# Kernel optimization log

Hardware: AMD Instinct MI355X
Metric: run time of the kernel (lower is better)

The kernel has to match this reference:

```python
import jax, jax.numpy as jnp
import numpy as np

L = 4            # num_layers
N_GENES = 2048   # col_dim: rows of x, PPI graph nodes
N_CELLS = 2048   # row_dim: cols of x, KNN graph nodes
E_KNN = 30720    # ~k=15 per cell
E_PPI = 65536    # ~avg degree 32 per gene
NEG_SLOPE = 0.01 # nn.LeakyReLU default


def setup_inputs() -> dict:
    key = jax.random.key(0)
    ks = jax.random.split(key, 9)
    x = jax.random.normal(ks[0], (N_GENES, N_CELLS), jnp.float32)
    knn_edge_index = jax.random.randint(ks[1], (2, E_KNN), 0, N_CELLS)
    ppi_edge_index = jax.random.randint(ks[2], (2, E_PPI), 0, N_GENES)
    s_c = 1.0 / np.sqrt(N_GENES)  # cols side feature dim = col_dim
    s_r = 1.0 / np.sqrt(N_CELLS)  # rows side feature dim = row_dim
    col_Wl = jax.random.normal(ks[3], (L, N_GENES, N_GENES), jnp.float32) * s_c
    col_bl = jnp.zeros((L, N_GENES), jnp.float32)
    col_Wr = jax.random.normal(ks[4], (L, N_GENES, N_GENES), jnp.float32) * s_c
    row_Wl = jax.random.normal(ks[5], (L, N_CELLS, N_CELLS), jnp.float32) * s_r
    row_bl = jnp.zeros((L, N_CELLS), jnp.float32)
    row_Wr = jax.random.normal(ks[6], (L, N_CELLS, N_CELLS), jnp.float32) * s_r
    return dict(x=x, knn_edge_index=knn_edge_index, ppi_edge_index=ppi_edge_index,
                col_Wl=col_Wl, col_bl=col_bl, col_Wr=col_Wr,
                row_Wl=row_Wl, row_bl=row_bl, row_Wr=row_Wr)


def _sage(h, edge_index, Wl, bl, Wr):
    # PyG SAGEConv (mean aggr): out = lin_l(mean_{j->i} h_j) + lin_r(h_i)
    src, tgt = edge_index[0], edge_index[1]
    n = h.shape[0]
    summed = jax.ops.segment_sum(h[src], tgt, num_segments=n)          # [n, d]
    cnt = jax.ops.segment_sum(jnp.ones((src.shape[0],), h.dtype), tgt, num_segments=n)
    mean = summed / jnp.maximum(cnt, 1.0)[:, None]
    return mean @ Wl + bl + h @ Wr


def reference(x, knn_edge_index, ppi_edge_index,
              col_Wl, col_bl, col_Wr, row_Wl, row_bl, row_Wr):
    # Dropout is identity in eval mode; layer = SAGEConv -> LeakyReLU on both sides.
    h = x  # [N_GENES, N_CELLS]
    for i in range(L):
        # cols side: operate on h.T [N_CELLS, N_GENES] over KNN graph
        h = jax.nn.leaky_relu(_sage(h.T, knn_edge_index, col_Wl[i], col_bl[i], col_Wr[i]),
                              negative_slope=NEG_SLOPE).T
        # rows side: operate on h [N_GENES, N_CELLS] over PPI graph
        h = jax.nn.leaky_relu(_sage(h, ppi_edge_index, row_Wl[i], row_bl[i], row_Wr[i]),
                              negative_slope=NEG_SLOPE)
    return h
```

## Files before the change

kernel.cpp:

```cpp
#include <hip/hip_runtime.h>
#include <stdint.h>

#define NSZ 2048
#define NLAYERS 4

typedef __attribute__((ext_vector_type(4))) float f32x4;
typedef __attribute__((ext_vector_type(4))) _Float16 f16x4;
typedef __attribute__((ext_vector_type(8))) _Float16 f16x8;

__device__ __forceinline__ void gload_lds16(const void* g, void* l) {
  __builtin_amdgcn_global_load_lds((const __attribute__((address_space(1))) void*)g,
                                   (__attribute__((address_space(3))) void*)l, 16, 0, 0);
}

__global__ void k_zero(int* __restrict__ p, int n) {
  int i = blockIdx.x * 256 + threadIdx.x;
  if (i < n) p[i] = 0;
}

__global__ void k_count(const int* __restrict__ tgt, int E, int* __restrict__ cnt) {
  int e = blockIdx.x * 256 + threadIdx.x;
  if (e < E) atomicAdd(&cnt[tgt[e] & (NSZ - 1)], 1);
}

__global__ __launch_bounds__(1024) void k_scan(
    const int* __restrict__ cntA, int* __restrict__ offA, int* __restrict__ curA,
    float* __restrict__ invA, int EA,
    const int* __restrict__ cntB, int* __restrict__ offB, int* __restrict__ curB,
    float* __restrict__ invB, int EB) {
  const int* cnt; int* off; int* cur; float* inv; int E;
  if (blockIdx.x == 0) { cnt = cntA; off = offA; cur = curA; inv = invA; E = EA; }
  else                 { cnt = cntB; off = offB; cur = curB; inv = invB; E = EB; }
  __shared__ int sa[2048], sb[2048];
  int t = threadIdx.x;
  sa[t] = cnt[t]; sa[t + 1024] = cnt[t + 1024];
  __syncthreads();
  int* s = sa; int* d = sb;
  for (int dd = 1; dd < 2048; dd <<= 1) {
    for (int i = t; i < 2048; i += 1024)
      d[i] = s[i] + ((i >= dd) ? s[i - dd] : 0);
    __syncthreads();
    int* tmp = s; s = d; d = tmp;
  }
  for (int i = t; i < 2048; i += 1024) {
    int o = (i == 0) ? 0 : s[i - 1];
    off[i] = o; cur[i] = o;
    int c = cnt[i];
    inv[i] = 1.0f / (float)((c > 1) ? c : 1);
  }
  if (t == 0) off[2048] = E;
}

__global__ void k_fill(const int* __restrict__ src, const int* __restrict__ tgt, int E,
                       int* __restrict__ cur, int* __restrict__ srcs) {
  int e = blockIdx.x * 256 + threadIdx.x;
  if (e < E) {
    int p = atomicAdd(&cur[tgt[e] & (NSZ - 1)], 1);
    if (p >= 0 && p < E) srcs[p] = src[e] & (NSZ - 1);
  }
}

__global__ __launch_bounds__(256) void k_transpose(const float* __restrict__ s,
                                                   float* __restrict__ d) {
  __shared__ float tile[64][65];
  const int tid = threadIdx.x;
  const int r0 = blockIdx.y << 6, c0 = blockIdx.x << 6;
#pragma unroll
  for (int it = 0; it < 4; ++it) {
    int e = it * 256 + tid;
    int r = e >> 4;
    int c = (e & 15) << 2;
    f32x4 v = *(const f32x4*)&s[(size_t)(r0 + r) * NSZ + c0 + c];
#pragma unroll
    for (int j = 0; j < 4; ++j) tile[r][c + j] = v[j];
  }
  __syncthreads();
#pragma unroll
  for (int it = 0; it < 4; ++it) {
    int e = it * 256 + tid;
    int r = e >> 4;
    int c = (e & 15) << 2;
    f32x4 v;
#pragma unroll
    for (int j = 0; j < 4; ++j) v[j] = tile[c + j][r];
    *(f32x4*)&d[(size_t)(c0 + r) * NSZ + r0 + c] = v;
  }
}

__global__ __launch_bounds__(256) void k_cvtA(const float* __restrict__ X,
                                              _Float16* __restrict__ Ah,
                                              _Float16* __restrict__ Al) {
  int idx = blockIdx.x * 256 + threadIdx.x;
  int m = idx >> 9;
  int c = idx & 511;
  f32x4 v = *(const f32x4*)&X[((size_t)m << 11) + (c << 2)];
  f16x4 hi, lo;
#pragma unroll
  for (int j = 0; j < 4; ++j) {
    float x = v[j];
    _Float16 h = (_Float16)x;
    hi[j] = h;
    lo[j] = (_Float16)(x - (float)h);
  }
  size_t rowb = (size_t)m << 12;
  int byte = (c << 3) ^ (((m >> 1) & 3) << 4);
  *(f16x4*)((char*)Ah + rowb + byte) = hi;
  *(f16x4*)((char*)Al + rowb + byte) = lo;
}

__global__ __launch_bounds__(256) void k_cvtB(const float* __restrict__ Wl,
                                              const float* __restrict__ Wr,
                                              _Float16* __restrict__ Bh,
                                              _Float16* __restrict__ Bl) {
  __shared__ float tile[64][65];
  const float* W = blockIdx.z ? Wr : Wl;
  const int nbase = blockIdx.z ? NSZ : 0;
  const int tid = threadIdx.x;
  const int k0 = blockIdx.y << 6;
  const int n0 = blockIdx.x << 6;
#pragma unroll
  for (int it = 0; it < 4; ++it) {
    int e = it * 256 + tid;
    int r = e >> 4;
    int c = (e & 15) << 2;
    f32x4 v = *(const f32x4*)&W[(size_t)(k0 + r) * NSZ + n0 + c];
#pragma unroll
    for (int j = 0; j < 4; ++j) tile[r][c + j] = v[j];
  }
  __syncthreads();
#pragma unroll
  for (int it = 0; it < 4; ++it) {
    int e = it * 256 + tid;
    int r = e >> 4;
    int c4 = (e & 15) << 2;
    f16x4 hi, lo;
#pragma unroll
    for (int j = 0; j < 4; ++j) {
      float x = tile[c4 + j][r];
      _Float16 h = (_Float16)x;
      hi[j] = h;
      lo[j] = (_Float16)(x - (float)h);
    }
    int n = nbase + n0 + r;
    size_t rowb = (size_t)n << 12;
    int byte = ((k0 + c4) << 1) ^ (((n >> 1) & 3) << 4);
    *(f16x4*)((char*)Bh + rowb + byte) = hi;
    *(f16x4*)((char*)Bl + rowb + byte) = lo;
  }
}

__global__ __launch_bounds__(256, 2) void k_gemm16(
    const _Float16* __restrict__ Ah, const _Float16* __restrict__ Al,
    const _Float16* __restrict__ Bh, const _Float16* __restrict__ Bl,
    float* __restrict__ C) {
  __shared__ __align__(128) _Float16 lds[4][128][32];
  const int tid = threadIdx.x;
  const int w = tid >> 6;
  const int lane = tid & 63;
  const int bm = blockIdx.x & 15;
  const int bn = blockIdx.x >> 4;
  const int m0 = bm << 7;
  const int n0 = bn << 7;
  const int wm = (w & 1) << 6;
  const int wn = (w >> 1) << 6;

  f32x4 acc[4][4];
#pragma unroll
  for (int i = 0; i < 4; ++i)
#pragma unroll
    for (int j = 0; j < 4; ++j)
#pragma unroll
      for (int r = 0; r < 4; ++r) acc[i][j][r] = 0.f;

  const int srow0 = (w << 5) + (lane >> 2);
  const int scol = (lane & 3) << 3;
  const int l15 = lane & 15;
  const int ks16 = (lane >> 4) << 4;

  for (int k0 = 0; k0 < NSZ; k0 += 32) {
    __syncthreads();
#pragma unroll
    for (int q = 0; q < 2; ++q) {
      const int r = srow0 + (q << 4);
      const int dr = ((w << 1) + q) << 4;
      gload_lds16(&Ah[(size_t)(m0 + r) * NSZ + k0 + scol], &lds[0][dr][0]);
      gload_lds16(&Al[(size_t)(m0 + r) * NSZ + k0 + scol], &lds[1][dr][0]);
      gload_lds16(&Bh[(size_t)(n0 + r) * NSZ + k0 + scol], &lds[2][dr][0]);
      gload_lds16(&Bl[(size_t)(n0 + r) * NSZ + k0 + scol], &lds[3][dr][0]);
    }
    __syncthreads();

    f16x8 afh[4], afl[4], bfh[4], bfl[4];
#pragma unroll
    for (int f = 0; f < 4; ++f) {
      const int ra = wm + (f << 4) + l15;
      const int ca = ks16 ^ (((ra >> 1) & 3) << 4);
      afh[f] = *(const f16x8*)((const char*)&lds[0][ra][0] + ca);
      afl[f] = *(const f16x8*)((const char*)&lds[1][ra][0] + ca);
      const int rb = wn + (f << 4) + l15;
      const int cb = ks16 ^ (((rb >> 1) & 3) << 4);
      bfh[f] = *(const f16x8*)((const char*)&lds[2][rb][0] + cb);
      bfl[f] = *(const f16x8*)((const char*)&lds[3][rb][0] + cb);
    }
#pragma unroll
    for (int i = 0; i < 4; ++i)
#pragma unroll
      for (int j = 0; j < 4; ++j) {
        acc[i][j] = __builtin_amdgcn_mfma_f32_16x16x32_f16(afh[i], bfh[j], acc[i][j], 0, 0, 0);
        acc[i][j] = __builtin_amdgcn_mfma_f32_16x16x32_f16(afh[i], bfl[j], acc[i][j], 0, 0, 0);
        acc[i][j] = __builtin_amdgcn_mfma_f32_16x16x32_f16(afl[i], bfh[j], acc[i][j], 0, 0, 0);
      }
  }

  const int cr = (lane >> 4) << 2;
#pragma unroll
  for (int i = 0; i < 4; ++i)
#pragma unroll
    for (int j = 0; j < 4; ++j) {
      float* Cp = &C[(size_t)(m0 + wm + (i << 4) + cr) * 4096 + n0 + wn + (j << 4) + l15];
#pragma unroll
      for (int r = 0; r < 4; ++r) Cp[(size_t)r * 4096] = acc[i][j][r];
    }
}

__global__ __launch_bounds__(256) void k_fuse(const float* __restrict__ Cb,
                                              const int* __restrict__ off,
                                              const int* __restrict__ srcs,
                                              const float* __restrict__ inv,
                                              const float* __restrict__ bias,
                                              float* __restrict__ out,
                                              int transpose_out, int E) {
  __shared__ float tile[64][65];
  const int tid = threadIdx.x;
  const int w = tid >> 6;
  const int lane = tid & 63;
  const int t0 = blockIdx.y << 6;
  const int f0 = blockIdx.x << 6;
  const int fc = f0 + lane;
  const float b = bias[fc];

  for (int it = 0; it < 16; ++it) {
    int lt = (w << 4) + it;
    int c = t0 + lt;
    int e0 = off[c], e1 = off[c + 1];
    if (e1 > E) e1 = E;
    if (e0 < 0) e0 = 0;
    float acc = 0.f;
    int e = e0;
    while (e + 8 <= e1) {
      float p[8];
#pragma unroll
      for (int q = 0; q < 8; ++q)
        p[q] = Cb[(size_t)(srcs[e + q] & (NSZ - 1)) * 4096 + fc];
#pragma unroll
      for (int q = 0; q < 8; ++q) acc += p[q];
      e += 8;
    }
    while (e < e1) { acc += Cb[(size_t)(srcs[e] & (NSZ - 1)) * 4096 + fc]; ++e; }
    float val = acc * inv[c] + Cb[(size_t)c * 4096 + 2048 + fc] + b;
    val = (val > 0.f) ? val : 0.01f * val;
    tile[lt][lane] = val;
  }
  __syncthreads();
  for (int it = 0; it < 4; ++it) {
    int f = it * 256 + tid;
    int r = f >> 4;
    int c4 = (f & 15) << 2;
    f32x4 v;
    if (transpose_out) {
#pragma unroll
      for (int j = 0; j < 4; ++j) v[j] = tile[c4 + j][r];
      *(f32x4*)&out[(size_t)(f0 + r) * NSZ + t0 + c4] = v;
    } else {
#pragma unroll
      for (int j = 0; j < 4; ++j) v[j] = tile[r][c4 + j];
      *(f32x4*)&out[(size_t)(t0 + r) * NSZ + f0 + c4] = v;
    }
  }
}

extern "C" void kernel_launch(void* const* d_in, const int* in_sizes, int n_in,
                              void* d_out, int out_size, void* d_ws, size_t ws_size,
                              hipStream_t stream) {
  (void)n_in; (void)out_size; (void)ws_size;
  const float* x      = (const float*)d_in[0];
  const int*   knn    = (const int*)d_in[1];
  const int*   ppi    = (const int*)d_in[2];
  const float* col_Wl = (const float*)d_in[3];
  const float* col_bl = (const float*)d_in[4];
  const float* col_Wr = (const float*)d_in[5];
  const float* row_Wl = (const float*)d_in[6];
  const float* row_bl = (const float*)d_in[7];
  const float* row_Wr = (const float*)d_in[8];
  float* out = (float*)d_out;
  const int E_knn = in_sizes[1] / 2;
  const int E_ppi = in_sizes[2] / 2;
  const size_t NN = (size_t)NSZ * NSZ;

  char* ws = (char*)d_ws;
  size_t off_b = 0;
  int*   cnt_knn = (int*)(ws + off_b);   off_b += 2048 * 4;
  int*   cnt_ppi = (int*)(ws + off_b);   off_b += 2048 * 4;
  int*   off_knn = (int*)(ws + off_b);   off_b += 2064 * 4;
  int*   off_ppi = (int*)(ws + off_b);   off_b += 2064 * 4;
  int*   cur_knn = (int*)(ws + off_b);   off_b += 2048 * 4;
  int*   cur_ppi = (int*)(ws + off_b);   off_b += 2048 * 4;
  float* inv_knn = (float*)(ws + off_b); off_b += 2048 * 4;
  float* inv_ppi = (float*)(ws + off_b); off_b += 2048 * 4;
  int*   src_knn = (int*)(ws + off_b);   off_b += (size_t)((E_knn + 63) & ~63) * 4;
  int*   src_ppi = (int*)(ws + off_b);   off_b += (size_t)((E_ppi + 63) & ~63) * 4;
  off_b = (off_b + 255) & ~(size_t)255;
  float*     Cbuf = (float*)(ws + off_b);     off_b += NN * 2 * 4;
  _Float16*  Ahw  = (_Float16*)(ws + off_b);  off_b += NN * 2;
  _Float16*  Alw  = (_Float16*)(ws + off_b);  off_b += NN * 2;
  _Float16*  Bhw  = (_Float16*)(ws + off_b);  off_b += NN * 2 * 2;
  _Float16*  Blw  = (_Float16*)(ws + off_b);  off_b += NN * 2 * 2;
  float* state = out;

  k_zero<<<16, 256, 0, stream>>>(cnt_knn, 4096);
  k_count<<<(E_knn + 255) / 256, 256, 0, stream>>>(knn + E_knn, E_knn, cnt_knn);
  k_count<<<(E_ppi + 255) / 256, 256, 0, stream>>>(ppi + E_ppi, E_ppi, cnt_ppi);
  k_scan<<<2, 1024, 0, stream>>>(cnt_knn, off_knn, cur_knn, inv_knn, E_knn,
                                 cnt_ppi, off_ppi, cur_ppi, inv_ppi, E_ppi);
  k_fill<<<(E_knn + 255) / 256, 256, 0, stream>>>(knn, knn + E_knn, E_knn, cur_knn, src_knn);
  k_fill<<<(E_ppi + 255) / 256, 256, 0, stream>>>(ppi, ppi + E_ppi, E_ppi, cur_ppi, src_ppi);

  {
    dim3 g(32, 32);
    k_transpose<<<g, 256, 0, stream>>>(x, state);
  }

  for (int i = 0; i < NLAYERS; ++i) {
    dim3 gf(32, 32);
    dim3 gb(32, 32, 2);
    k_cvtA<<<4096, 256, 0, stream>>>(state, Ahw, Alw);
    k_cvtB<<<gb, 256, 0, stream>>>(col_Wl + (size_t)i * NN, col_Wr + (size_t)i * NN, Bhw, Blw);
    k_gemm16<<<512, 256, 0, stream>>>(Ahw, Alw, Bhw, Blw, Cbuf);
    k_fuse<<<gf, 256, 0, stream>>>(Cbuf, off_knn, src_knn, inv_knn,
                                   col_bl + (size_t)i * NSZ, state, 1, E_knn);
    k_cvtA<<<4096, 256, 0, stream>>>(state, Ahw, Alw);
    k_cvtB<<<gb, 256, 0, stream>>>(row_Wl + (size_t)i * NN, row_Wr + (size_t)i * NN, Bhw, Blw);
    k_gemm16<<<512, 256, 0, stream>>>(Ahw, Alw, Bhw, Blw, Cbuf);
    k_fuse<<<gf, 256, 0, stream>>>(Cbuf, off_ppi, src_ppi, inv_ppi,
                                   row_bl + (size_t)i * NSZ, out,
                                   (i < NLAYERS - 1) ? 1 : 0, E_ppi);
  }
}
```

Baseline: 1.694 ms.

## Fuse fp16 split conversion into transpose/fuse epilogues and double-buffer GEMM LDS

The initial transpose and the per-layer fuse epilogues now write the hi/lo fp16 split operands directly in the swizzled layout the GEMM expects. This removes the separate k_cvtA passes and the fp32 state round-trip through global memory. The GEMM gains a double-buffered LDS stage, so the next K tile's global-to-LDS loads are issued before the MFMAs, and one barrier per iteration is dropped. Block indices are also remapped to change the tile visiting order for cache locality. The cost is twice the LDS per block, which may reduce occupancy below the launch-bounds target.

```diff
diff --git a/kernel.cpp b/kernel.cpp
--- a/kernel.cpp
+++ b/kernel.cpp
@@ -60,8 +60,9 @@
   }
 }
 
-__global__ __launch_bounds__(256) void k_transpose(const float* __restrict__ s,
-                                                   float* __restrict__ d) {
+__global__ __launch_bounds__(256) void k_transpose_cvt(const float* __restrict__ s,
+                                                       _Float16* __restrict__ Ah,
+                                                       _Float16* __restrict__ Al) {
   __shared__ float tile[64][65];
   const int tid = threadIdx.x;
   const int r0 = blockIdx.y << 6, c0 = blockIdx.x << 6;
@@ -79,33 +80,21 @@
   for (int it = 0; it < 4; ++it) {
     int e = it * 256 + tid;
     int r = e >> 4;
-    int c = (e & 15) << 2;
-    f32x4 v;
-#pragma unroll
-    for (int j = 0; j < 4; ++j) v[j] = tile[c + j][r];
-    *(f32x4*)&d[(size_t)(c0 + r) * NSZ + r0 + c] = v;
-  }
-}
-
-__global__ __launch_bounds__(256) void k_cvtA(const float* __restrict__ X,
-                                              _Float16* __restrict__ Ah,
-                                              _Float16* __restrict__ Al) {
-  int idx = blockIdx.x * 256 + threadIdx.x;
-  int m = idx >> 9;
-  int c = idx & 511;
-  f32x4 v = *(const f32x4*)&X[((size_t)m << 11) + (c << 2)];
-  f16x4 hi, lo;
-#pragma unroll
-  for (int j = 0; j < 4; ++j) {
-    float x = v[j];
-    _Float16 h = (_Float16)x;
-    hi[j] = h;
-    lo[j] = (_Float16)(x - (float)h);
-  }
-  size_t rowb = (size_t)m << 12;
-  int byte = (c << 3) ^ (((m >> 1) & 3) << 4);
-  *(f16x4*)((char*)Ah + rowb + byte) = hi;
-  *(f16x4*)((char*)Al + rowb + byte) = lo;
+    int c4 = (e & 15) << 2;
+    f16x4 hi, lo;
+#pragma unroll
+    for (int j = 0; j < 4; ++j) {
+      float x = tile[c4 + j][r];
+      _Float16 h = (_Float16)x;
+      hi[j] = h;
+      lo[j] = (_Float16)(x - (float)h);
+    }
+    int m = c0 + r;
+    size_t rowb = (size_t)m << 12;
+    int byte = ((r0 + c4) << 1) ^ (((m >> 1) & 3) << 4);
+    *(f16x4*)((char*)Ah + rowb + byte) = hi;
+    *(f16x4*)((char*)Al + rowb + byte) = lo;
+  }
 }
 
 __global__ __launch_bounds__(256) void k_cvtB(const float* __restrict__ Wl,
@@ -153,12 +142,14 @@
     const _Float16* __restrict__ Ah, const _Float16* __restrict__ Al,
     const _Float16* __restrict__ Bh, const _Float16* __restrict__ Bl,
     float* __restrict__ C) {
-  __shared__ __align__(128) _Float16 lds[4][128][32];
+  __shared__ __align__(128) _Float16 lds[2][4][128][32];
   const int tid = threadIdx.x;
   const int w = tid >> 6;
   const int lane = tid & 63;
-  const int bm = blockIdx.x & 15;
-  const int bn = blockIdx.x >> 4;
+  int bid = blockIdx.x;
+  bid = ((bid & 7) << 6) | (bid >> 3);
+  const int bm = bid & 15;
+  const int bn = bid >> 4;
   const int m0 = bm << 7;
   const int n0 = bn << 7;
   const int wm = (w & 1) << 6;
@@ -177,30 +168,40 @@
   const int l15 = lane & 15;
   const int ks16 = (lane >> 4) << 4;
 
+  const size_t aoff = (size_t)(m0 + srow0) * NSZ + scol;
+  const size_t boff = (size_t)(n0 + srow0) * NSZ + scol;
+
+#define STAGE(buf, kk)                                                     \
+  do {                                                                     \
+    _Pragma("unroll") for (int q = 0; q < 2; ++q) {                        \
+      const size_t go = (size_t)(q << 4) * NSZ + (kk);                     \
+      const int dr = ((w << 1) + q) << 4;                                  \
+      gload_lds16(&Ah[aoff + go], &lds[buf][0][dr][0]);                    \
+      gload_lds16(&Al[aoff + go], &lds[buf][1][dr][0]);                    \
+      gload_lds16(&Bh[boff + go], &lds[buf][2][dr][0]);                    \
+      gload_lds16(&Bl[boff + go], &lds[buf][3][dr][0]);                    \
+    }                                                                      \
+  } while (0)
+
+  STAGE(0, 0);
+  __syncthreads();
+
+  int cur = 0;
   for (int k0 = 0; k0 < NSZ; k0 += 32) {
-    __syncthreads();
-#pragma unroll
-    for (int q = 0; q < 2; ++q) {
-      const int r = srow0 + (q << 4);
-      const int dr = ((w << 1) + q) << 4;
-      gload_lds16(&Ah[(size_t)(m0 + r) * NSZ + k0 + scol], &lds[0][dr][0]);
-      gload_lds16(&Al[(size_t)(m0 + r) * NSZ + k0 + scol], &lds[1][dr][0]);
-      gload_lds16(&Bh[(size_t)(n0 + r) * NSZ + k0 + scol], &lds[2][dr][0]);
-      gload_lds16(&Bl[(size_t)(n0 + r) * NSZ + k0 + scol], &lds[3][dr][0]);
-    }
-    __syncthreads();
+    const int nxt = cur ^ 1;
+    if (k0 + 32 < NSZ) STAGE(nxt, k0 + 32);
 
     f16x8 afh[4], afl[4], bfh[4], bfl[4];
 #pragma unroll
     for (int f = 0; f < 4; ++f) {
       const int ra = wm + (f << 4) + l15;
       const int ca = ks16 ^ (((ra >> 1) & 3) << 4);
-      afh[f] = *(const f16x8*)((const char*)&lds[0][ra][0] + ca);
-      afl[f] = *(const f16x8*)((const char*)&lds[1][ra][0] + ca);
+      afh[f] = *(const f16x8*)((const char*)&lds[cur][0][ra][0] + ca);
+      afl[f] = *(const f16x8*)((const char*)&lds[cur][1][ra][0] + ca);
       const int rb = wn + (f << 4) + l15;
       const int cb = ks16 ^ (((rb >> 1) & 3) << 4);
-      bfh[f] = *(const f16x8*)((const char*)&lds[2][rb][0] + cb);
-      bfl[f] = *(const f16x8*)((const char*)&lds[3][rb][0] + cb);
+      bfh[f] = *(const f16x8*)((const char*)&lds[cur][2][rb][0] + cb);
+      bfl[f] = *(const f16x8*)((const char*)&lds[cur][3][rb][0] + cb);
     }
 #pragma unroll
     for (int i = 0; i < 4; ++i)
@@ -210,7 +211,10 @@
         acc[i][j] = __builtin_amdgcn_mfma_f32_16x16x32_f16(afh[i], bfl[j], acc[i][j], 0, 0, 0);
         acc[i][j] = __builtin_amdgcn_mfma_f32_16x16x32_f16(afl[i], bfh[j], acc[i][j], 0, 0, 0);
       }
-  }
+    __syncthreads();
+    cur = nxt;
+  }
+#undef STAGE
 
   const int cr = (lane >> 4) << 2;
 #pragma unroll
@@ -228,8 +232,10 @@
                                               const int* __restrict__ srcs,
                                               const float* __restrict__ inv,
                                               const float* __restrict__ bias,
-                                              float* __restrict__ out,
-                                              int transpose_out, int E) {
+                                              float* __restrict__ outF,
+                                              _Float16* __restrict__ oh,
+                                              _Float16* __restrict__ ol,
+                                              int mode, int E) {
   __shared__ float tile[64][65];
   const int tid = threadIdx.x;
   const int w = tid >> 6;
@@ -266,15 +272,25 @@
     int f = it * 256 + tid;
     int r = f >> 4;
     int c4 = (f & 15) << 2;
-    f32x4 v;
-    if (transpose_out) {
-#pragma unroll
-      for (int j = 0; j < 4; ++j) v[j] = tile[c4 + j][r];
-      *(f32x4*)&out[(size_t)(f0 + r) * NSZ + t0 + c4] = v;
+    if (mode) {
+      f16x4 hi, lo;
+#pragma unroll
+      for (int j = 0; j < 4; ++j) {
+        float x = tile[c4 + j][r];
+        _Float16 h = (_Float16)x;
+        hi[j] = h;
+        lo[j] = (_Float16)(x - (float)h);
+      }
+      int m = f0 + r;
+      size_t rowb = (size_t)m << 12;
+      int byte = ((t0 + c4) << 1) ^ (((m >> 1) & 3) << 4);
+      *(f16x4*)((char*)oh + rowb + byte) = hi;
+      *(f16x4*)((char*)ol + rowb + byte) = lo;
     } else {
+      f32x4 v;
 #pragma unroll
       for (int j = 0; j < 4; ++j) v[j] = tile[r][c4 + j];
-      *(f32x4*)&out[(size_t)(t0 + r) * NSZ + f0 + c4] = v;
+      *(f32x4*)&outF[(size_t)(t0 + r) * NSZ + f0 + c4] = v;
     }
   }
 }
@@ -315,7 +331,6 @@
   _Float16*  Alw  = (_Float16*)(ws + off_b);  off_b += NN * 2;
   _Float16*  Bhw  = (_Float16*)(ws + off_b);  off_b += NN * 2 * 2;
   _Float16*  Blw  = (_Float16*)(ws + off_b);  off_b += NN * 2 * 2;
-  float* state = out;
 
   k_zero<<<16, 256, 0, stream>>>(cnt_knn, 4096);
   k_count<<<(E_knn + 255) / 256, 256, 0, stream>>>(knn + E_knn, E_knn, cnt_knn);
@@ -327,22 +342,20 @@
 
   {
     dim3 g(32, 32);
-    k_transpose<<<g, 256, 0, stream>>>(x, state);
+    k_transpose_cvt<<<g, 256, 0, stream>>>(x, Ahw, Alw);
   }
 
   for (int i = 0; i < NLAYERS; ++i) {
     dim3 gf(32, 32);
     dim3 gb(32, 32, 2);
-    k_cvtA<<<4096, 256, 0, stream>>>(state, Ahw, Alw);
     k_cvtB<<<gb, 256, 0, stream>>>(col_Wl + (size_t)i * NN, col_Wr + (size_t)i * NN, Bhw, Blw);
     k_gemm16<<<512, 256, 0, stream>>>(Ahw, Alw, Bhw, Blw, Cbuf);
     k_fuse<<<gf, 256, 0, stream>>>(Cbuf, off_knn, src_knn, inv_knn,
-                                   col_bl + (size_t)i * NSZ, state, 1, E_knn);
-    k_cvtA<<<4096, 256, 0, stream>>>(state, Ahw, Alw);
+                                   col_bl + (size_t)i * NSZ, out, Ahw, Alw, 1, E_knn);
     k_cvtB<<<gb, 256, 0, stream>>>(row_Wl + (size_t)i * NN, row_Wr + (size_t)i * NN, Bhw, Blw);
     k_gemm16<<<512, 256, 0, stream>>>(Ahw, Alw, Bhw, Blw, Cbuf);
     k_fuse<<<gf, 256, 0, stream>>>(Cbuf, off_ppi, src_ppi, inv_ppi,
-                                   row_bl + (size_t)i * NSZ, out,
+                                   row_bl + (size_t)i * NSZ, out, Ahw, Alw,
                                    (i < NLAYERS - 1) ? 1 : 0, E_ppi);
   }
 }
```

Measured after the change: 1.598 ms. 1.06x faster.
